# Kernel optimization log

Measured on AMD Instinct MI355X. Metric: run time of the kernel, lower is better.

Reference implementation:

```python
import jax, jax.numpy as jnp
import numpy as np

NUM_HEADS = 16


def setup_inputs() -> dict:
    key = jax.random.key(0)
    ks = jax.random.split(key, 8)
    B, W, D = 128, 512, 2048
    s = 1.0 / np.sqrt(D)
    return {
        "x": jax.random.normal(ks[0], (B, D), jnp.float32),
        "buffer": jax.random.normal(ks[1], (B, W, D), jnp.float32),
        "Wq": jax.random.normal(ks[2], (D, D), jnp.float32) * s,
        "Wk": jax.random.normal(ks[3], (D, D), jnp.float32) * s,
        "Wv": jax.random.normal(ks[4], (D, D), jnp.float32) * s,
        "Wo": jax.random.normal(ks[5], (D, D), jnp.float32) * s,
        "Wg": jax.random.normal(ks[6], (D, 2 * D), jnp.float32) * (1.0 / np.sqrt(2 * D)),
        "bg": jnp.zeros((D,), jnp.float32),
    }


def reference(x, buffer, Wq, Wk, Wv, Wo, Wg, bg):
    B, D = x.shape
    H = NUM_HEADS
    Dh = D // H
    scale = Dh ** -0.5
    # steady-state ring buffer update: roll left, append x at last slot
    kv_seq = jnp.concatenate([buffer[:, 1:], x[:, None, :]], axis=1)  # [B, W, D]
    # projections (nn.Linear: y = x @ W.T)
    q = (x @ Wq.T).reshape(B, H, Dh)                      # [B, H, Dh]
    k = (kv_seq @ Wk.T).reshape(B, -1, H, Dh)             # [B, W, H, Dh]
    v = (kv_seq @ Wv.T).reshape(B, -1, H, Dh)
    # single-query attention over the window
    logits = jnp.einsum("bhd,bshd->bhs", q, k) * scale    # [B, H, W]
    attn = jax.nn.softmax(logits, axis=-1)
    out = jnp.einsum("bhs,bshd->bhd", attn, v).reshape(B, D)
    out = out @ Wo.T
    # gated residual
    g = jax.nn.sigmoid(jnp.concatenate([x, out], axis=-1) @ Wg.T + bg)
    return x + g * out
```

## Files before the change

### kernel.cpp

```cpp
#include <hip/hip_runtime.h>
#include <hip/hip_bf16.h>
#include <math.h>

#define B_   128
#define W_   512
#define D_   2048
#define H_   16
#define DH_  128

typedef __attribute__((ext_vector_type(4))) float f32x4;
typedef __attribute__((ext_vector_type(8))) short bf16x8;

typedef const __attribute__((address_space(1))) void* gvp;
typedef __attribute__((address_space(3))) void* lvp;

__device__ inline short f2bf(float f) {
  union { __hip_bfloat16 h; short s; } u;
  u.h = __float2bfloat16(f);
  return u.s;
}
__device__ inline float bf2f(unsigned short u) {
  return __uint_as_float(((unsigned)u) << 16);
}

#define LGKM_BARRIER() do {                                   \
    asm volatile("s_waitcnt lgkmcnt(0)" ::: "memory");        \
    __builtin_amdgcn_sched_barrier(0);                        \
    __builtin_amdgcn_s_barrier();                             \
    __builtin_amdgcn_sched_barrier(0);                        \
  } while (0)

template<bool BBF16, int AMODE>
__global__ __launch_bounds__(256) void gemm_mfma(
    const float* __restrict__ A, int a_rs, long a_hs,
    const float* __restrict__ A2, int a2_k,
    const void* __restrict__ Bv, int b_rs, long b_hs,
    float* __restrict__ C, int c_rs, long c_hs, long c_ks,
    int Kblk)
{
  __shared__ char sm[2][24576];

  const int t  = threadIdx.x;
  const int w  = t >> 6, l = t & 63, lo = l & 15, hi = l >> 4;
  const int wm = w >> 1, wn = w & 1;
  const int n0   = blockIdx.x * 64;
  const int head = blockIdx.y;
  const int ks   = blockIdx.z;
  const int kbeg = ks * Kblk;
  const int nit  = Kblk >> 6;

  const float* Ab = nullptr;
  if (AMODE == 0) {
    const float* base = A;
    int koff = kbeg;
    if (A2 && kbeg >= a2_k) { base = A2; koff = kbeg - a2_k; }
    Ab = base + head * a_hs + koff;
  }
  const float*          Bf = (const float*)Bv          + (BBF16 ? 0 : head * b_hs + (long)n0 * b_rs + kbeg);
  const unsigned short* Bh = (const unsigned short*)Bv + (BBF16 ? head * b_hs + (long)n0 * b_rs + kbeg : 0);

  const int ar = t >> 2;
  const int ak = (t & 3) * 16;

  f32x4 acc[4][2] = {};

  auto load_tiles = [&](int it, float4* ar4, float4* br4) {
    if (AMODE == 0) {
      const float* Ait = Ab + it * 64;
#pragma unroll
      for (int p = 0; p < 2; ++p) {
        const float* src = Ait + (long)(p * 64 + ar) * a_rs + ak;
#pragma unroll
        for (int qq = 0; qq < 4; ++qq) ar4[p * 4 + qq] = *(const float4*)(src + qq * 4);
      }
    } else {
      const unsigned short* pa = (const unsigned short*)A;
      const float* mlp = A2;
      const int col = kbeg + it * 64 + ak;
#pragma unroll
      for (int p = 0; p < 2; ++p) {
        int m  = p * 64 + ar;
        int bh = m * 16 + head;
        float m0 = mlp[bh * 2],              l0 = mlp[bh * 2 + 1];
        float m1 = mlp[(2048 + bh) * 2],     l1 = mlp[(2048 + bh) * 2 + 1];
        float M  = fmaxf(m0, m1);
        float w0 = __expf(m0 - M), w1 = __expf(m1 - M);
        float inv = 1.0f / (w0 * l0 + w1 * l1);
        w0 *= inv; w1 *= inv;
        const unsigned short* r0 = pa + (long)bh * D_ + col;
        const unsigned short* r1 = r0 + (long)B_ * H_ * D_;
#pragma unroll
        for (int q2 = 0; q2 < 2; ++q2) {
          bf16x8 a0 = *(const bf16x8*)(r0 + q2 * 8);
          bf16x8 a1 = *(const bf16x8*)(r1 + q2 * 8);
          float out[8];
#pragma unroll
          for (int j = 0; j < 8; ++j)
            out[j] = w0 * bf2f((unsigned short)a0[j]) + w1 * bf2f((unsigned short)a1[j]);
          ar4[p * 4 + q2 * 2]     = make_float4(out[0], out[1], out[2], out[3]);
          ar4[p * 4 + q2 * 2 + 1] = make_float4(out[4], out[5], out[6], out[7]);
        }
      }
    }
    if (BBF16) {
      const char* src = (const char*)(Bh + (long)ar * b_rs + it * 64 + ak);
      br4[0] = *(const float4*)(src);
      br4[1] = *(const float4*)(src + 16);
    } else {
      const float* src = Bf + (long)ar * b_rs + it * 64 + ak;
#pragma unroll
      for (int qq = 0; qq < 4; ++qq) br4[qq] = *(const float4*)(src + qq * 4);
    }
  };

  auto write_tiles = [&](int buf, const float4* ar4, const float4* br4) {
    char* As = sm[buf];
    char* Bs = sm[buf] + 16384;
#pragma unroll
    for (int p = 0; p < 2; ++p) {
      int m = p * 64 + ar;
      int base = m * 128 + ak * 2;
      int swz = (m & 7) << 4;
#pragma unroll
      for (int h2 = 0; h2 < 2; ++h2) {
        bf16x8 v;
        const float* f = (const float*)(ar4 + p * 4);
#pragma unroll
        for (int j = 0; j < 8; ++j) v[j] = f2bf(f[h2 * 8 + j]);
        *(bf16x8*)(As + ((base + h2 * 16) ^ swz)) = v;
      }
    }
    {
      int n = ar;
      int base = n * 128 + ak * 2;
      int swz = (n & 7) << 4;
      if (BBF16) {
#pragma unroll
        for (int h2 = 0; h2 < 2; ++h2)
          *(bf16x8*)(Bs + ((base + h2 * 16) ^ swz)) = ((const bf16x8*)br4)[h2];
      } else {
#pragma unroll
        for (int h2 = 0; h2 < 2; ++h2) {
          bf16x8 v;
          const float* f = (const float*)br4;
#pragma unroll
          for (int j = 0; j < 8; ++j) v[j] = f2bf(f[h2 * 8 + j]);
          *(bf16x8*)(Bs + ((base + h2 * 16) ^ swz)) = v;
        }
      }
    }
  };

  auto compute = [&](int buf) {
    const char* As = sm[buf];
    const char* Bs = sm[buf] + 16384;
#pragma unroll
    for (int kk = 0; kk < 2; ++kk) {
      bf16x8 af[4], bfr[2];
#pragma unroll
      for (int mi = 0; mi < 4; ++mi) {
        int m = wm * 64 + mi * 16 + lo;
        af[mi] = *(const bf16x8*)(As + ((m * 128 + (kk * 32 + hi * 8) * 2) ^ ((m & 7) << 4)));
      }
#pragma unroll
      for (int ni = 0; ni < 2; ++ni) {
        int n = wn * 32 + ni * 16 + lo;
        bfr[ni] = *(const bf16x8*)(Bs + ((n * 128 + (kk * 32 + hi * 8) * 2) ^ ((n & 7) << 4)));
      }
#pragma unroll
      for (int mi = 0; mi < 4; ++mi)
#pragma unroll
        for (int ni = 0; ni < 2; ++ni)
          acc[mi][ni] = __builtin_amdgcn_mfma_f32_16x16x32_bf16(af[mi], bfr[ni], acc[mi][ni], 0, 0, 0);
    }
  };

  float4 ar4[8], br4[4];
  load_tiles(0, ar4, br4);
  write_tiles(0, ar4, br4);
  __syncthreads();
  for (int it = 0; it < nit; ++it) {
    float4 na[8], nb[4];
    if (it + 1 < nit) load_tiles(it + 1, na, nb);
    compute(it & 1);
    if (it + 1 < nit) write_tiles((it + 1) & 1, na, nb);
    __syncthreads();
  }

  float* Cb = C + c_ks * ks + c_hs * head + n0;
#pragma unroll
  for (int mi = 0; mi < 4; ++mi)
#pragma unroll
    for (int ni = 0; ni < 2; ++ni)
#pragma unroll
      for (int r = 0; r < 4; ++r)
        Cb[(long)(wm * 64 + mi * 16 + hi * 4 + r) * c_rs + (wn * 32 + ni * 16 + lo)] = acc[mi][ni][r];
}

__global__ __launch_bounds__(256) void transpose_wk(
    const float* __restrict__ Wk, unsigned short* __restrict__ WkT)
{
  __shared__ float tile[64][68];
  const int t  = threadIdx.x;
  const int e0 = blockIdx.x * 64;
  const int d0 = blockIdx.y * 64;
  const int h  = blockIdx.z;
  {
    int d = t >> 2, eq = (t & 3) * 16;
    const float* src = Wk + (long)(h * DH_ + d0 + d) * D_ + e0 + eq;
#pragma unroll
    for (int qq = 0; qq < 4; ++qq)
      *(float4*)&tile[d][eq + qq * 4] = *(const float4*)(src + qq * 4);
  }
  __syncthreads();
  {
    int e = t >> 2, dq = (t & 3) * 16;
    unsigned short* dst = WkT + ((long)h * D_ + e0 + e) * DH_ + d0 + dq;
    bf16x8 v0, v1;
#pragma unroll
    for (int j = 0; j < 8; ++j) v0[j] = f2bf(tile[dq + j][e]);
#pragma unroll
    for (int j = 0; j < 8; ++j) v1[j] = f2bf(tile[dq + 8 + j][e]);
    *(bf16x8*)dst = v0;
    *(bf16x8*)(dst + 8) = v1;
  }
}

__global__ void reduce_add_k(const float* __restrict__ part, int ns, long stride,
                             long n, float* __restrict__ out)
{
  for (long i = (long)blockIdx.x * blockDim.x + threadIdx.x; i < n;
       i += (long)gridDim.x * blockDim.x) {
    float s = 0.f;
    for (int k = 0; k < ns; ++k) s += part[k * stride + i];
    out[i] = s;
  }
}

__global__ __launch_bounds__(1024, 4) void fused_attn(
    const float* __restrict__ x, const float* __restrict__ buffer,
    const float* __restrict__ qt, unsigned short* __restrict__ part,
    float* __restrict__ ml)
{
  __shared__ float kv[2 * 8 * 2048];
  __shared__ float lacc[16][9][20];
  __shared__ float pbuf[16][8];
  __shared__ float sbuf[16];

  const int b    = blockIdx.x;
  const int half = blockIdx.y;
  const int t    = threadIdx.x;
  const int w    = t >> 6;
  const int lane = t & 63;
  const int lo   = lane & 15;
  const int hi   = lane >> 4;
  const char* kvb = (const char*)kv;

  bf16x8 afrag[4];
  {
    const float* qrow = qt + ((long)b * H_ + lo) * D_;
    const float sc = 0.088388347648318447f;
#pragma unroll
    for (int kk = 0; kk < 4; ++kk) {
      int e0 = w * 128 + kk * 32 + hi * 8;
#pragma unroll
      for (int j = 0; j < 8; ++j) afrag[kk][j] = f2bf(qrow[e0 + j] * sc);
    }
  }

  float accE[16][2];
#pragma unroll
  for (int h = 0; h < 16; ++h) { accE[h][0] = 0.f; accE[h][1] = 0.f; }
  float m_run = -1e30f, l_run = 0.f;

  auto stage = [&](int sb, int tl) {
#pragma unroll
    for (int r = 0; r < 4; ++r) {
      int s = r * 2 + (w >> 3);
      int inrow = (w & 7) * 1024 + lane * 16;
      int srco = inrow ^ (s << 4);
      int s_glob = half * 256 + tl * 8 + s;
      const float* row = (s_glob < W_ - 1)
          ? buffer + (((long)(b * W_ + s_glob + 1)) << 11)
          : x + ((long)b << 11);
      __builtin_amdgcn_global_load_lds(
          (gvp)(row + (srco >> 2)),
          (lvp)(kv + sb * 16384 + r * 4096 + w * 256), 16, 0, 0);
    }
  };

  stage(0, 0);
  __syncthreads();

  for (int tile = 0; tile < 32; ++tile) {
    const int buf  = tile & 1;
    const int bufo = buf * 65536;

    if (tile + 1 < 32) stage(buf ^ 1, tile + 1);

    {
      f32x4 c4 = {0.f, 0.f, 0.f, 0.f};
      const int srow = lo & 7;
#pragma unroll
      for (int kk = 0; kk < 4; ++kk) {
        unsigned B0 = (unsigned)(srow * 8192 + (w * 128 + kk * 32 + hi * 8) * 4);
        unsigned o1 = B0 ^ (unsigned)(srow << 4);
        float4 f1 = *(const float4*)(kvb + bufo + o1);
        float4 f2 = *(const float4*)(kvb + bufo + (o1 ^ 16u));
        unsigned u[4];
        u[0] = __builtin_amdgcn_perm(__float_as_uint(f1.y), __float_as_uint(f1.x), 0x07060302u);
        u[1] = __builtin_amdgcn_perm(__float_as_uint(f1.w), __float_as_uint(f1.z), 0x07060302u);
        u[2] = __builtin_amdgcn_perm(__float_as_uint(f2.y), __float_as_uint(f2.x), 0x07060302u);
        u[3] = __builtin_amdgcn_perm(__float_as_uint(f2.w), __float_as_uint(f2.z), 0x07060302u);
        bf16x8 bf;
        __builtin_memcpy(&bf, u, 16);
        c4 = __builtin_amdgcn_mfma_f32_16x16x32_bf16(afrag[kk], bf, c4, 0, 0, 0);
      }
      if (lo < 8) *(f32x4*)&lacc[w][lo][hi * 4] = c4;
    }

    float2 kvp[8];
    {
      const unsigned ebyte = (unsigned)((w * 128 + lane * 2) * 4);
#pragma unroll
      for (int s = 0; s < 8; ++s) {
        unsigned Bx = (unsigned)(s * 8192) + ebyte;
        kvp[s] = *(const float2*)(kvb + bufo + (Bx ^ (unsigned)(s << 4)));
      }
    }
    LGKM_BARRIER();

    {
      const int s   = lane & 7;
      const int wwg = lane >> 3;
      float v = lacc[wwg][s][w] + lacc[wwg + 8][s][w];
      v += __shfl_xor(v, 8);
      v += __shfl_xor(v, 16);
      v += __shfl_xor(v, 32);
      float mt = v;
      mt = fmaxf(mt, __shfl_xor(mt, 1));
      mt = fmaxf(mt, __shfl_xor(mt, 2));
      mt = fmaxf(mt, __shfl_xor(mt, 4));
      float m_new = fmaxf(m_run, mt);
      float scl = __expf(m_run - m_new);
      float p = __expf(v - m_new);
      float ps = p;
      ps += __shfl_xor(ps, 1);
      ps += __shfl_xor(ps, 2);
      ps += __shfl_xor(ps, 4);
      l_run = l_run * scl + ps;
      m_run = m_new;
      if (lane < 8) pbuf[w][lane] = p;
      if (lane == 0) sbuf[w] = scl;
    }
    LGKM_BARRIER();

#pragma unroll
    for (int h = 0; h < 16; ++h) {
      float scl = sbuf[h];
      float a0 = accE[h][0] * scl, a1 = accE[h][1] * scl;
      float4 pA = *(const float4*)&pbuf[h][0];
      float4 pB = *(const float4*)&pbuf[h][4];
      a0 += pA.x * kvp[0].x + pA.y * kvp[1].x + pA.z * kvp[2].x + pA.w * kvp[3].x
          + pB.x * kvp[4].x + pB.y * kvp[5].x + pB.z * kvp[6].x + pB.w * kvp[7].x;
      a1 += pA.x * kvp[0].y + pA.y * kvp[1].y + pA.z * kvp[2].y + pA.w * kvp[3].y
          + pB.x * kvp[4].y + pB.y * kvp[5].y + pB.z * kvp[6].y + pB.w * kvp[7].y;
      accE[h][0] = a0; accE[h][1] = a1;
    }
    __syncthreads();
  }

  {
    long base = ((long)half * B_ + b) * H_;
#pragma unroll
    for (int h = 0; h < 16; ++h) {
      long idx = (base + h) * D_ + w * 128 + lane * 2;
      unsigned u0 = (unsigned short)f2bf(accE[h][0]);
      unsigned u1 = (unsigned short)f2bf(accE[h][1]);
      *(unsigned*)(part + idx) = u0 | (u1 << 16);
    }
    if (lane == 0) {
      ml[(base + w) * 2 + 0] = m_run;
      ml[(base + w) * 2 + 1] = l_run;
    }
  }
}

__global__ __launch_bounds__(256) void gate_final_k(
    const float* __restrict__ part, const float* __restrict__ bg,
    const float* __restrict__ x, const float* __restrict__ out1,
    float* __restrict__ y)
{
  const long i = (long)blockIdx.x * 256 + threadIdx.x;
  float z = bg[i & (D_ - 1)];
#pragma unroll
  for (int k = 0; k < 8; ++k) z += part[(long)k * (B_ * D_) + i];
  const float g = 1.0f / (1.0f + expf(-z));
  y[i] = x[i] + g * out1[i];
}

extern "C" void kernel_launch(void* const* d_in, const int* in_sizes, int n_in,
                              void* d_out, int out_size, void* d_ws, size_t ws_size,
                              hipStream_t stream)
{
  const float* x      = (const float*)d_in[0];
  const float* buffer = (const float*)d_in[1];
  const float* Wq     = (const float*)d_in[2];
  const float* Wk     = (const float*)d_in[3];
  const float* Wv     = (const float*)d_in[4];
  const float* Wo     = (const float*)d_in[5];
  const float* Wg     = (const float*)d_in[6];
  const float* bg     = (const float*)d_in[7];
  float* y = (float*)d_out;

  float* ws    = (float*)d_ws;
  float* q     = ws;
  float* qt    = ws + 262144;
  unsigned short* part_a = (unsigned short*)(ws + 4456448);
  float* ml    = ws + 8650752;
  float* o0    = ws + 8658944;
  float* o1    = ws + 8921088;
  float* partg = ws + 9183232;
  unsigned short* wkT = (unsigned short*)(ws + 11280384);

  const long S = (long)B_ * D_;

  transpose_wk<<<dim3(32, 2, 16), 256, 0, stream>>>(Wk, wkT);

  gemm_mfma<false, 0><<<dim3(32, 1, 8), 256, 0, stream>>>(
      x, D_, 0, nullptr, 1 << 30, Wq, D_, 0, partg, D_, 0, S, 256);
  reduce_add_k<<<512, 256, 0, stream>>>(partg, 8, S, S, q);

  gemm_mfma<true, 0><<<dim3(32, 16, 1), 256, 0, stream>>>(
      q, D_, DH_, nullptr, 1 << 30, wkT, DH_, (long)D_ * DH_,
      qt, H_ * D_, D_, 0, DH_);

  fused_attn<<<dim3(B_, 2), 1024, 0, stream>>>(x, buffer, qt, part_a, ml);

  gemm_mfma<false, 1><<<dim3(2, 16, 8), 256, 0, stream>>>(
      (const float*)part_a, 0, 0, ml, 0, Wv, D_, (long)DH_ * D_,
      partg, D_, DH_, S, 256);
  reduce_add_k<<<512, 256, 0, stream>>>(partg, 8, S, S, o0);

  gemm_mfma<false, 0><<<dim3(32, 1, 8), 256, 0, stream>>>(
      o0, D_, 0, nullptr, 1 << 30, Wo, D_, 0, partg, D_, 0, S, 256);
  reduce_add_k<<<512, 256, 0, stream>>>(partg, 8, S, S, o1);

  gemm_mfma<false, 0><<<dim3(32, 1, 8), 256, 0, stream>>>(
      x, D_, 0, o1, D_, Wg, 2 * D_, 0, partg, D_, 0, S, 512);
  gate_final_k<<<1024, 256, 0, stream>>>(partg, bg, x, o1, y);

  (void)in_sizes; (void)n_in; (void)out_size; (void)ws_size;
}
```

Baseline: 244.8 us.

## Software-pipeline softmax weights so PV accumulation lags one tile, removing a barrier

```diff
diff --git a/kernel.cpp b/kernel.cpp
--- a/kernel.cpp
+++ b/kernel.cpp
@@ -244,8 +244,8 @@
 {
   __shared__ float kv[2 * 8 * 2048];
   __shared__ float lacc[16][9][20];
-  __shared__ float pbuf[16][8];
-  __shared__ float sbuf[16];
+  __shared__ float pbuf[2][16][8];
+  __shared__ float sbuf[2][16];
 
   const int b    = blockIdx.x;
   const int half = blockIdx.y;
@@ -289,15 +289,9 @@
     }
   };
 
-  stage(0, 0);
-  __syncthreads();
-
-  for (int tile = 0; tile < 32; ++tile) {
-    const int buf  = tile & 1;
+  auto phase1 = [&](int tile, int buf, float2* kvpCur) {
     const int bufo = buf * 65536;
-
     if (tile + 1 < 32) stage(buf ^ 1, tile + 1);
-
     {
       f32x4 c4 = {0.f, 0.f, 0.f, 0.f};
       const int srow = lo & 7;
@@ -318,18 +312,17 @@
       }
       if (lo < 8) *(f32x4*)&lacc[w][lo][hi * 4] = c4;
     }
-
-    float2 kvp[8];
     {
       const unsigned ebyte = (unsigned)((w * 128 + lane * 2) * 4);
 #pragma unroll
       for (int s = 0; s < 8; ++s) {
         unsigned Bx = (unsigned)(s * 8192) + ebyte;
-        kvp[s] = *(const float2*)(kvb + bufo + (Bx ^ (unsigned)(s << 4)));
-      }
-    }
-    LGKM_BARRIER();
-
+        kvpCur[s] = *(const float2*)(kvb + bufo + (Bx ^ (unsigned)(s << 4)));
+      }
+    }
+  };
+
+  auto phase2 = [&](int tile, int slot, const float2* kvpPrev) {
     {
       const int s   = lane & 7;
       const int wwg = lane >> 3;
@@ -350,24 +343,55 @@
       ps += __shfl_xor(ps, 4);
       l_run = l_run * scl + ps;
       m_run = m_new;
-      if (lane < 8) pbuf[w][lane] = p;
-      if (lane == 0) sbuf[w] = scl;
-    }
+      if (lane < 8) pbuf[slot][w][lane] = p;
+      if (lane == 0) sbuf[slot][w] = scl;
+    }
+    if (tile > 0) {
+      const int sp = slot ^ 1;
+#pragma unroll
+      for (int h = 0; h < 16; ++h) {
+        float scl = sbuf[sp][h];
+        float a0 = accE[h][0] * scl, a1 = accE[h][1] * scl;
+        float4 pA = *(const float4*)&pbuf[sp][h][0];
+        float4 pB = *(const float4*)&pbuf[sp][h][4];
+        a0 += pA.x * kvpPrev[0].x + pA.y * kvpPrev[1].x + pA.z * kvpPrev[2].x + pA.w * kvpPrev[3].x
+            + pB.x * kvpPrev[4].x + pB.y * kvpPrev[5].x + pB.z * kvpPrev[6].x + pB.w * kvpPrev[7].x;
+        a1 += pA.x * kvpPrev[0].y + pA.y * kvpPrev[1].y + pA.z * kvpPrev[2].y + pA.w * kvpPrev[3].y
+            + pB.x * kvpPrev[4].y + pB.y * kvpPrev[5].y + pB.z * kvpPrev[6].y + pB.w * kvpPrev[7].y;
+        accE[h][0] = a0; accE[h][1] = a1;
+      }
+    }
+  };
+
+  stage(0, 0);
+  __syncthreads();
+
+  float2 kvpA[8], kvpB[8];
+  for (int it2 = 0; it2 < 16; ++it2) {
+    const int t0 = it2 * 2;
+    phase1(t0, 0, kvpA);
     LGKM_BARRIER();
-
+    phase2(t0, 0, kvpB);
+    __syncthreads();
+    phase1(t0 + 1, 1, kvpB);
+    LGKM_BARRIER();
+    phase2(t0 + 1, 1, kvpA);
+    __syncthreads();
+  }
+
+  {
 #pragma unroll
     for (int h = 0; h < 16; ++h) {
-      float scl = sbuf[h];
+      float scl = sbuf[1][h];
       float a0 = accE[h][0] * scl, a1 = accE[h][1] * scl;
-      float4 pA = *(const float4*)&pbuf[h][0];
-      float4 pB = *(const float4*)&pbuf[h][4];
-      a0 += pA.x * kvp[0].x + pA.y * kvp[1].x + pA.z * kvp[2].x + pA.w * kvp[3].x
-          + pB.x * kvp[4].x + pB.y * kvp[5].x + pB.z * kvp[6].x + pB.w * kvp[7].x;
-      a1 += pA.x * kvp[0].y + pA.y * kvp[1].y + pA.z * kvp[2].y + pA.w * kvp[3].y
-          + pB.x * kvp[4].y + pB.y * kvp[5].y + pB.z * kvp[6].y + pB.w * kvp[7].y;
+      float4 pA = *(const float4*)&pbuf[1][h][0];
+      float4 pB = *(const float4*)&pbuf[1][h][4];
+      a0 += pA.x * kvpB[0].x + pA.y * kvpB[1].x + pA.z * kvpB[2].x + pA.w * kvpB[3].x
+          + pB.x * kvpB[4].x + pB.y * kvpB[5].x + pB.z * kvpB[6].x + pB.w * kvpB[7].x;
+      a1 += pA.x * kvpB[0].y + pA.y * kvpB[1].y + pA.z * kvpB[2].y + pA.w * kvpB[3].y
+          + pB.x * kvpB[4].y + pB.y * kvpB[5].y + pB.z * kvpB[6].y + pB.w * kvpB[7].y;
       accE[h][0] = a0; accE[h][1] = a1;
     }
-    __syncthreads();
   }
 
   {
```

Result: slower. 309.6 us (+26.5%).

## Fuse split-K partial reductions into consumer GEMM A-loads and gate kernel

Applied to the files above, without the earlier changes.

```diff
diff --git a/kernel.cpp b/kernel.cpp
--- a/kernel.cpp
+++ b/kernel.cpp
@@ -7,6 +7,7 @@
 #define D_   2048
 #define H_   16
 #define DH_  128
+#define SLC_ 262144
 
 typedef __attribute__((ext_vector_type(4))) float f32x4;
 typedef __attribute__((ext_vector_type(8))) short bf16x8;
@@ -50,11 +51,18 @@
   const int nit  = Kblk >> 6;
 
   const float* Ab = nullptr;
+  bool sum8 = false;
   if (AMODE == 0) {
     const float* base = A;
     int koff = kbeg;
     if (A2 && kbeg >= a2_k) { base = A2; koff = kbeg - a2_k; }
     Ab = base + head * a_hs + koff;
+  } else if (AMODE == 2) {
+    Ab = A + head * a_hs + kbeg;
+    sum8 = true;
+  } else if (AMODE == 3) {
+    if (kbeg < a2_k) { Ab = A + kbeg; sum8 = false; }
+    else            { Ab = A2 + (kbeg - a2_k); sum8 = true; }
   }
   const float*          Bf = (const float*)Bv          + (BBF16 ? 0 : head * b_hs + (long)n0 * b_rs + kbeg);
   const unsigned short* Bh = (const unsigned short*)Bv + (BBF16 ? head * b_hs + (long)n0 * b_rs + kbeg : 0);
@@ -65,13 +73,21 @@
   f32x4 acc[4][2] = {};
 
   auto load_tiles = [&](int it, float4* ar4, float4* br4) {
-    if (AMODE == 0) {
+    if (AMODE != 1) {
       const float* Ait = Ab + it * 64;
 #pragma unroll
       for (int p = 0; p < 2; ++p) {
         const float* src = Ait + (long)(p * 64 + ar) * a_rs + ak;
 #pragma unroll
-        for (int qq = 0; qq < 4; ++qq) ar4[p * 4 + qq] = *(const float4*)(src + qq * 4);
+        for (int qq = 0; qq < 4; ++qq) {
+          f32x4 v = *(const f32x4*)(src + qq * 4);
+          if (AMODE >= 2 && sum8) {
+#pragma unroll
+            for (int s = 1; s < 8; ++s)
+              v += *(const f32x4*)(src + (long)s * SLC_ + qq * 4);
+          }
+          ar4[p * 4 + qq] = *(const float4*)&v;
+        }
       }
     } else {
       const unsigned short* pa = (const unsigned short*)A;
@@ -223,17 +239,6 @@
     for (int j = 0; j < 8; ++j) v1[j] = f2bf(tile[dq + 8 + j][e]);
     *(bf16x8*)dst = v0;
     *(bf16x8*)(dst + 8) = v1;
-  }
-}
-
-__global__ void reduce_add_k(const float* __restrict__ part, int ns, long stride,
-                             long n, float* __restrict__ out)
-{
-  for (long i = (long)blockIdx.x * blockDim.x + threadIdx.x; i < n;
-       i += (long)gridDim.x * blockDim.x) {
-    float s = 0.f;
-    for (int k = 0; k < ns; ++k) s += part[k * stride + i];
-    out[i] = s;
   }
 }
 
@@ -387,16 +392,20 @@
 }
 
 __global__ __launch_bounds__(256) void gate_final_k(
-    const float* __restrict__ part, const float* __restrict__ bg,
-    const float* __restrict__ x, const float* __restrict__ out1,
+    const float* __restrict__ pg6, const float* __restrict__ p3,
+    const float* __restrict__ bg, const float* __restrict__ x,
     float* __restrict__ y)
 {
   const long i = (long)blockIdx.x * 256 + threadIdx.x;
   float z = bg[i & (D_ - 1)];
-#pragma unroll
-  for (int k = 0; k < 8; ++k) z += part[(long)k * (B_ * D_) + i];
+  float o = 0.f;
+#pragma unroll
+  for (int k = 0; k < 8; ++k) {
+    z += pg6[(long)k * SLC_ + i];
+    o += p3[(long)k * SLC_ + i];
+  }
   const float g = 1.0f / (1.0f + expf(-z));
-  y[i] = x[i] + g * out1[i];
+  y[i] = x[i] + g * o;
 }
 
 extern "C" void kernel_launch(void* const* d_in, const int* in_sizes, int n_in,
@@ -414,41 +423,38 @@
   float* y = (float*)d_out;
 
   float* ws    = (float*)d_ws;
-  float* q     = ws;
-  float* qt    = ws + 262144;
-  unsigned short* part_a = (unsigned short*)(ws + 4456448);
-  float* ml    = ws + 8650752;
-  float* o0    = ws + 8658944;
-  float* o1    = ws + 8921088;
-  float* partg = ws + 9183232;
-  unsigned short* wkT = (unsigned short*)(ws + 11280384);
-
-  const long S = (long)B_ * D_;
+  float* qt    = ws;
+  float* partg3 = ws;
+  float* pg6   = ws + 2097152;
+  unsigned short* part_a = (unsigned short*)(ws + 4194304);
+  float* ml    = ws + 8388608;
+  float* pgA   = ws + 8396800;
+  unsigned short* wkT = (unsigned short*)(ws + 10493952);
+
+  const long S = (long)SLC_;
 
   transpose_wk<<<dim3(32, 2, 16), 256, 0, stream>>>(Wk, wkT);
 
   gemm_mfma<false, 0><<<dim3(32, 1, 8), 256, 0, stream>>>(
-      x, D_, 0, nullptr, 1 << 30, Wq, D_, 0, partg, D_, 0, S, 256);
-  reduce_add_k<<<512, 256, 0, stream>>>(partg, 8, S, S, q);
-
-  gemm_mfma<true, 0><<<dim3(32, 16, 1), 256, 0, stream>>>(
-      q, D_, DH_, nullptr, 1 << 30, wkT, DH_, (long)D_ * DH_,
+      x, D_, 0, nullptr, 1 << 30, Wq, D_, 0, pgA, D_, 0, S, 256);
+
+  gemm_mfma<true, 2><<<dim3(32, 16, 1), 256, 0, stream>>>(
+      pgA, D_, DH_, nullptr, 0, wkT, DH_, (long)D_ * DH_,
       qt, H_ * D_, D_, 0, DH_);
 
   fused_attn<<<dim3(B_, 2), 1024, 0, stream>>>(x, buffer, qt, part_a, ml);
 
   gemm_mfma<false, 1><<<dim3(2, 16, 8), 256, 0, stream>>>(
       (const float*)part_a, 0, 0, ml, 0, Wv, D_, (long)DH_ * D_,
-      partg, D_, DH_, S, 256);
-  reduce_add_k<<<512, 256, 0, stream>>>(partg, 8, S, S, o0);
-
-  gemm_mfma<false, 0><<<dim3(32, 1, 8), 256, 0, stream>>>(
-      o0, D_, 0, nullptr, 1 << 30, Wo, D_, 0, partg, D_, 0, S, 256);
-  reduce_add_k<<<512, 256, 0, stream>>>(partg, 8, S, S, o1);
-
-  gemm_mfma<false, 0><<<dim3(32, 1, 8), 256, 0, stream>>>(
-      x, D_, 0, o1, D_, Wg, 2 * D_, 0, partg, D_, 0, S, 512);
-  gate_final_k<<<1024, 256, 0, stream>>>(partg, bg, x, o1, y);
+      pgA, D_, DH_, S, 256);
+
+  gemm_mfma<false, 2><<<dim3(32, 1, 8), 256, 0, stream>>>(
+      pgA, D_, 0, nullptr, 0, Wo, D_, 0, partg3, D_, 0, S, 256);
+
+  gemm_mfma<false, 3><<<dim3(32, 1, 8), 256, 0, stream>>>(
+      x, D_, 0, partg3, D_, Wg, 2 * D_, 0, pg6, D_, 0, S, 512);
+
+  gate_final_k<<<1024, 256, 0, stream>>>(pg6, partg3, bg, x, y);
 
   (void)in_sizes; (void)n_in; (void)out_size; (void)ws_size;
 }
```

Result: slower. 315.9 us (+29.1%).
